# Kernel optimization log

Hardware: AMD Instinct MI355X
Metric: run time of the kernel (lower is better)

## Reference

```python
import jax, jax.numpy as jnp
import numpy as np

N, E = 50000, 800000
FN, FE, D, H = 64, 16, 128, 4


def setup_inputs() -> dict:
    key = jax.random.key(0)
    ks = jax.random.split(key, 16)
    inp = {
        "nodes": jax.random.normal(ks[0], (N, FN), jnp.float32),
        "edges": jax.random.normal(ks[1], (E, FE), jnp.float32),
        "senders": jax.random.randint(ks[2], (E,), 0, N, jnp.int32),
        "receivers": jax.random.randint(ks[3], (E,), 0, N, jnp.int32),
        "avg_multi_head": 0,
        # params (orthogonal init approximated by scaled normal; math identical)
        "W_node": jax.random.normal(ks[4], (FN, D), jnp.float32) / np.sqrt(FN),
        "b_node": jnp.zeros((D,), jnp.float32),
        "W_edge": jax.random.normal(ks[5], (FE, D), jnp.float32) / np.sqrt(FE),
        "b_edge": jnp.zeros((D,), jnp.float32),
        "Wk_s": jax.random.normal(ks[6], (H, D, D), jnp.float32) / np.sqrt(D),
        "bk_s": jnp.zeros((H, D), jnp.float32),
        "Wk_r": jax.random.normal(ks[7], (H, D, D), jnp.float32) / np.sqrt(D),
        "bk_r": jnp.zeros((H, D), jnp.float32),
        "W_out": jax.random.normal(ks[8], (H * D, D), jnp.float32) / np.sqrt(H * D),
        "b_out": jnp.zeros((D,), jnp.float32),
    }
    return inp


def _segment_softmax(logits, seg_ids, num_segments):
    seg_max = jax.ops.segment_max(logits, seg_ids, num_segments=num_segments)
    seg_max = jnp.where(jnp.isfinite(seg_max), seg_max, 0.0)  # empty segments
    e = jnp.exp(logits - seg_max[seg_ids])
    seg_sum = jax.ops.segment_sum(e, seg_ids, num_segments=num_segments)
    return e / seg_sum[seg_ids]


def reference(nodes, edges, senders, receivers, avg_multi_head,
              W_node, b_node, W_edge, b_edge, Wk_s, bk_s, Wk_r, bk_r,
              W_out, b_out):
    n_node = nodes.shape[0]
    x = nodes @ W_node + b_node            # [N, D] projected nodes
    ef = edges @ W_edge + b_edge           # [E, D] projected edge features
    sa = x[senders]                        # [E, D] sent attributes
    ra = x[receivers]                      # [E, D] received attributes
    scale = 1.0 / jnp.sqrt(jnp.asarray(D, x.dtype))
    heads = []
    for h in range(H):  # small fixed head count, structurally distinct params
        k_s = sa @ Wk_s[h] + bk_s[h]                 # [E, D]
        k_r = ra @ Wk_r[h] + bk_r[h] + ef            # [E, D]
        logits = jnp.sum(k_s * k_r, axis=1) * scale  # [E]
        w = _segment_softmax(logits, receivers, n_node)
        msg = w[:, None] * (sa + ef)                 # [E, D]
        heads.append(jax.ops.segment_sum(msg, receivers, num_segments=n_node))
    if avg_multi_head:
        agg = jnp.mean(jnp.stack(heads), axis=0)
    else:
        agg = jnp.concatenate(heads, axis=1) @ W_out + b_out
    return jax.nn.relu(x + agg)            # new node features [N, D]
```

## Files before the change

### kernel.cpp

```cpp
#include <hip/hip_runtime.h>

typedef unsigned short u16;
typedef unsigned int u32;
typedef short bh8 __attribute__((ext_vector_type(8)));
typedef float f4 __attribute__((ext_vector_type(4)));
typedef float pf2 __attribute__((ext_vector_type(2)));

__device__ __forceinline__ float bf2f(u16 h) { return __uint_as_float(((u32)h) << 16); }
__device__ __forceinline__ float bflo(u32 u) { return __uint_as_float(u << 16); }
__device__ __forceinline__ float bfhi(u32 u) { return __uint_as_float(u & 0xffff0000u); }
__device__ __forceinline__ u16 f2bf(float f) {
    u32 x = __float_as_uint(f);
    return (u16)((x + 0x7fffu + ((x >> 16) & 1u)) >> 16);
}
__device__ __forceinline__ pf2 pkfma(pf2 a, pf2 b, pf2 c) {
    pf2 d;
    asm("v_pk_fma_f32 %0, %1, %2, %3" : "=v"(d) : "v"(a), "v"(b), "v"(c));
    return d;
}
__device__ __forceinline__ pf2 u2f2(u32 u) {
    pf2 r;
    r.x = bflo(u);
    r.y = bfhi(u);
    return r;
}
__device__ __forceinline__ float dpp_red16(float x) {
    int y;
    y = __builtin_amdgcn_update_dpp(0, __float_as_int(x), 0xB1, 0xF, 0xF, true);
    x += __int_as_float(y);
    y = __builtin_amdgcn_update_dpp(0, __float_as_int(x), 0x4E, 0xF, 0xF, true);
    x += __int_as_float(y);
    y = __builtin_amdgcn_update_dpp(0, __float_as_int(x), 0x141, 0xF, 0xF, true);
    x += __int_as_float(y);
    y = __builtin_amdgcn_update_dpp(0, __float_as_int(x), 0x140, 0xF, 0xF, true);
    x += __int_as_float(y);
    return x;
}

#define KSCL 0.12751744336457488f

__global__ void k0a_kernel(const float* __restrict__ Wn, const float* __restrict__ Wks,
                           const float* __restrict__ Wkr, float* __restrict__ A,
                           float* __restrict__ B) {
    int idx = blockIdx.x * 256 + threadIdx.x;
    if (idx >= 65536) return;
    int which = idx >> 15;
    int rem = idx & 32767;
    int h = rem >> 13;
    int r = rem & 8191;
    int a = r >> 7, dp = r & 127;
    const float* W = which ? Wks : Wkr;
    float acc = 0.f;
    for (int d = 0; d < 128; ++d)
        acc += Wn[a * 128 + d] * W[(h * 128 + d) * 128 + dp];
    (which ? B : A)[(h * 64 + a) * 128 + dp] = acc;
}

__global__ void k0a2_kernel(const float* __restrict__ bn, const float* __restrict__ Wks,
                            const float* __restrict__ Wkr, const float* __restrict__ bks,
                            const float* __restrict__ bkr, float* __restrict__ ybs,
                            float* __restrict__ ybr) {
    int idx = blockIdx.x * 256 + threadIdx.x;
    if (idx >= 1024) return;
    int which = idx >> 9;
    int rem = idx & 511;
    int h = rem >> 7, dp = rem & 127;
    const float* W = which ? Wks : Wkr;
    const float* b = which ? bks : bkr;
    float acc = b[h * 128 + dp];
    for (int d = 0; d < 128; ++d) acc += bn[d] * W[(h * 128 + d) * 128 + dp];
    (which ? ybs : ybr)[h * 128 + dp] = acc;
}

__global__ void k0b_kernel(const float* __restrict__ Wn, const float* __restrict__ bn,
                           const float* __restrict__ A, const float* __restrict__ B,
                           const float* __restrict__ ybr, const float* __restrict__ ybs,
                           const float* __restrict__ Wks, const float* __restrict__ Wedge,
                           const float* __restrict__ bks, const float* __restrict__ bedge,
                           float* __restrict__ Wfold, float* __restrict__ biasrow) {
    int idx = blockIdx.x * 256 + threadIdx.x;
    if (idx >= 65 * 708) return;
    int a = idx / 708, c = idx % 708;
    float val;
    if (c < 128) {
        val = (a < 64) ? Wn[a * 128 + c] : bn[c];
    } else if (c < 640) {
        int h = (c - 128) >> 7, i = (c - 128) & 127;
        const float* rv = (a < 64) ? &A[(h * 64 + a) * 128] : &ybr[h * 128];
        float s = 0.f;
        for (int d = 0; d < 128; ++d) s += rv[d] * Wks[(h * 128 + i) * 128 + d];
        val = s;
    } else if (c < 704) {
        int k = (c - 640) >> 2, h = (c - 640) & 3;
        const float* rv = (a < 64) ? &B[(h * 64 + a) * 128] : &ybs[h * 128];
        float s = 0.f;
        for (int d = 0; d < 128; ++d) s += rv[d] * Wedge[k * 128 + d];
        val = s;
    } else {
        int h = c - 704;
        const float* rv = (a < 64) ? &B[(h * 64 + a) * 128] : &ybs[h * 128];
        float s = 0.f;
        for (int d = 0; d < 128; ++d) s += rv[d] * bedge[d];
        val = s;
    }
    if (a < 64) Wfold[(size_t)a * 708 + c] = val;
    else biasrow[c] = val;
}

__global__ void wconv_kernel(const float* __restrict__ Wfold, const float* __restrict__ Wout,
                             u16* __restrict__ WfT, u16* __restrict__ WoT) {
    int i = blockIdx.x * 256 + threadIdx.x;
    if (i < 768 * 64) {
        int c = i >> 6, k = i & 63;
        WfT[i] = f2bf(c < 708 ? Wfold[(size_t)k * 708 + c] : 0.f);
    }
    int j = i - 768 * 64;
    if (j >= 0 && j < 128 * 512) {
        int c = j >> 9, k = j & 511;
        WoT[j] = f2bf(Wout[(size_t)k * 128 + c]);
    }
}

__global__ __launch_bounds__(256) void g1_kernel(const float* __restrict__ nodes,
                                                 const u16* __restrict__ WfT,
                                                 const float* __restrict__ biasrow,
                                                 u16* __restrict__ Xc, u16* __restrict__ V,
                                                 u16* __restrict__ U, float* __restrict__ E0,
                                                 int N) {
    __shared__ u16 Asm[64][72];
    __shared__ u16 Bsm[128][72];
    int t = threadIdx.x;
    int r0 = blockIdx.x * 64, c0 = blockIdx.y * 128;
    {
        int row = t >> 2, cb = (t & 3) * 16;
        int r = r0 + row;
        u16 pk[16];
        if (r < N) {
            const float* src = &nodes[(size_t)r * 64 + cb];
#pragma unroll
            for (int q = 0; q < 16; ++q) pk[q] = f2bf(src[q]);
        } else {
#pragma unroll
            for (int q = 0; q < 16; ++q) pk[q] = 0;
        }
        *(uint4*)&Asm[row][cb] = *(const uint4*)&pk[0];
        *(uint4*)&Asm[row][cb + 8] = *(const uint4*)&pk[8];
    }
    {
        int col = t >> 1, ks = (t & 1) * 32;
        const u16* src = &WfT[(size_t)(c0 + col) * 64 + ks];
        uint4 v0 = *(const uint4*)src;
        uint4 v1 = *(const uint4*)(src + 8);
        uint4 v2 = *(const uint4*)(src + 16);
        uint4 v3 = *(const uint4*)(src + 24);
        *(uint4*)&Bsm[col][ks] = v0;
        *(uint4*)&Bsm[col][ks + 8] = v1;
        *(uint4*)&Bsm[col][ks + 16] = v2;
        *(uint4*)&Bsm[col][ks + 24] = v3;
    }
    __syncthreads();
    int lane = t & 63, wave = t >> 6;
    int wm = wave >> 1, wn = wave & 1;
    int lr = lane & 15, lk = lane >> 4;
    f4 acc[2][4] = {};
#pragma unroll
    for (int kk = 0; kk < 2; ++kk) {
        bh8 a[2], b[4];
#pragma unroll
        for (int am = 0; am < 2; ++am)
            a[am] = *(const bh8*)&Asm[wm * 32 + am * 16 + lr][kk * 32 + lk * 8];
#pragma unroll
        for (int bn = 0; bn < 4; ++bn)
            b[bn] = *(const bh8*)&Bsm[wn * 64 + bn * 16 + lr][kk * 32 + lk * 8];
#pragma unroll
        for (int am = 0; am < 2; ++am)
#pragma unroll
            for (int bn = 0; bn < 4; ++bn)
                acc[am][bn] = __builtin_amdgcn_mfma_f32_16x16x32_bf16(a[am], b[bn], acc[am][bn], 0, 0, 0);
    }
#pragma unroll
    for (int am = 0; am < 2; ++am)
#pragma unroll
        for (int bn = 0; bn < 4; ++bn) {
            int c = c0 + wn * 64 + bn * 16 + lr;
            if (c < 708) {
                float brow = biasrow[c];
#pragma unroll
                for (int q = 0; q < 4; ++q) {
                    int r = r0 + wm * 32 + am * 16 + lk * 4 + q;
                    if (r < N) {
                        float val = acc[am][bn][q] + brow;
                        if (c < 128) Xc[(size_t)r * 128 + c] = f2bf(val);
                        else if (c < 640) V[(size_t)r * 512 + (c - 128)] = f2bf(val * KSCL);
                        else if (c < 704) U[(size_t)r * 64 + (c - 640)] = f2bf(val * KSCL);
                        else E0[(size_t)r * 4 + (c - 704)] = exp2f(val * KSCL);
                    }
                }
            }
        }
}

__global__ void hist_kernel(const int* __restrict__ recv, int* __restrict__ deg, int E) {
    int e = blockIdx.x * 256 + threadIdx.x;
    if (e < E) atomicAdd(&deg[recv[e]], 1);
}

__global__ __launch_bounds__(1024) void scan1_kernel(const int* __restrict__ deg,
                                                     int* __restrict__ pre,
                                                     int* __restrict__ bsum, int N) {
    __shared__ int sm[1024];
    int b = blockIdx.x, t = threadIdx.x;
    int i = b * 1024 + t;
    int v = (i < N) ? deg[i] : 0;
    sm[t] = v;
    __syncthreads();
    for (int off = 1; off < 1024; off <<= 1) {
        int u = (t >= off) ? sm[t - off] : 0;
        __syncthreads();
        sm[t] += u;
        __syncthreads();
    }
    if (i < N) pre[i] = sm[t] - v;
    if (t == 1023) bsum[b] = sm[1023];
}

__global__ void scan2_kernel(int* __restrict__ bsum, int* __restrict__ boff, int nb) {
    int t = threadIdx.x;
    int own = (t < nb) ? bsum[t] : 0;
    int v = own;
#pragma unroll
    for (int off = 1; off < 64; off <<= 1) {
        int u = __shfl_up(v, off);
        if (t >= off) v += u;
    }
    if (t < nb) boff[t] = v - own;
    if (t == 63) boff[64] = v;
}

__global__ void scan3_kernel(const int* __restrict__ pre, const int* __restrict__ boff,
                             int* __restrict__ row_start, int* __restrict__ cursor, int N) {
    int i = blockIdx.x * 1024 + threadIdx.x;
    if (i < N) {
        int rsv = pre[i] + boff[i >> 10];
        row_start[i] = rsv;
        cursor[i] = rsv;
    }
    if (i == N) row_start[N] = boff[64];
}

__global__ void scatter_kernel(const int* __restrict__ recv, const int* __restrict__ senders,
                               int* __restrict__ cursor, int2* __restrict__ esp, int E) {
    int e = blockIdx.x * 256 + threadIdx.x;
    if (e < E) {
        int s = senders[e];
        int p = atomicAdd(&cursor[recv[e]], 1);
        esp[p] = make_int2(e, s);
    }
}

__global__ __launch_bounds__(256, 4) void en_kernel(const int* __restrict__ row_start,
                                                    const int2* __restrict__ esp,
                                                    const float* __restrict__ edges,
                                                    const u16* __restrict__ Xc,
                                                    const u16* __restrict__ V,
                                                    const u16* __restrict__ Uu,
                                                    const float* __restrict__ E0,
                                                    const float* __restrict__ W_edge,
                                                    const float* __restrict__ b_edge,
                                                    u16* __restrict__ agg, int N) {
    __shared__ float Wl[2048];
    int t = threadIdx.x;
    for (int i = t; i < 2048; i += 256) {
        int k = i >> 7, ch = i & 127;
        int pos = (k << 7) | ((((ch >> 1) & 3) << 5) | (((ch >> 3) & 15) << 1) | (ch & 1));
        Wl[pos] = W_edge[i];
    }
    __syncthreads();
    int lane = t & 63, wid = t >> 6;
    int g = lane >> 4, k16 = lane & 15;
    int hp = wid & 1;
    int nw = blockIdx.x * 2 + (wid >> 1);
    int NW = gridDim.x * 2;

#define IDX8(ea, sa, eb, sb, s_)                                            \
    {                                                                       \
        int ev = 0, sv = 0;                                                 \
        if (lane < 8) {                                                     \
            int jj = (s_)*8 + lane;                                         \
            if (jj >= deg) jj = deg - 1;                                    \
            int2 pv = esp[rs + jj];                                         \
            ev = pv.x; sv = pv.y;                                           \
        }                                                                   \
        ea = __shfl(ev, g); sa = __shfl(sv, g);                             \
        eb = __shfl(ev, 4 + g); sb = __shfl(sv, 4 + g);                     \
    }

#define LOADP(Xq, Uq, Eq, Zq, eI, sI)                                       \
    {                                                                       \
        Xq = *(const uint4*)(Xc + (size_t)(sI)*128 + 8 * k16);              \
        Uq = *(const u32*)(Uu + (size_t)(sI)*64 + k16 * 4 + 2 * hp);        \
        Eq = edges[(size_t)(eI)*16 + k16];                                  \
        Zq = *(const float2*)(E0 + (size_t)(sI)*4 + 2 * hp);                \
    }

#define COMP(Xq, Uq, Eq, Zq, act)                                           \
    {                                                                       \
        pf2 X0 = u2f2(Xq.x), X1 = u2f2(Xq.y), X2 = u2f2(Xq.z), X3 = u2f2(Xq.w); \
        float uh0 = bflo(Uq), uh1 = bfhi(Uq);                               \
        pf2 p2 = {Eq * uh0, 0.f};                                           \
        p2 = pkfma(X0, v00, p2); p2 = pkfma(X1, v01, p2);                   \
        p2 = pkfma(X2, v02, p2); p2 = pkfma(X3, v03, p2);                   \
        float p = dpp_red16(p2.x + p2.y);                                   \
        float wh = (act) ? Zq.x * exp2f(p) : 0.f;                           \
        Ss0 += wh; aE0 = fmaf(wh, Eq, aE0);                                 \
        pf2 w2 = {wh, wh};                                                  \
        aX00 = pkfma(w2, X0, aX00); aX01 = pkfma(w2, X1, aX01);             \
        aX02 = pkfma(w2, X2, aX02); aX03 = pkfma(w2, X3, aX03);             \
        pf2 q2 = {Eq * uh1, 0.f};                                           \
        q2 = pkfma(X0, v10, q2); q2 = pkfma(X1, v11, q2);                   \
        q2 = pkfma(X2, v12, q2); q2 = pkfma(X3, v13, q2);                   \
        float q = dpp_red16(q2.x + q2.y);                                   \
        float wg = (act) ? Zq.y * exp2f(q) : 0.f;                           \
        Ss1 += wg; aE1 = fmaf(wg, Eq, aE1);                                 \
        pf2 g2 = {wg, wg};                                                  \
        aX10 = pkfma(g2, X0, aX10); aX11 = pkfma(g2, X1, aX11);             \
        aX12 = pkfma(g2, X2, aX12); aX13 = pkfma(g2, X3, aX13);             \
    }

    for (int n = nw; n < N; n += NW) {
        int rs = row_start[n];
        int deg = row_start[n + 1] - rs;
        const u16* Vr = V + (size_t)n * 512;
        pf2 v00, v01, v02, v03, v10, v11, v12, v13;
        {
            uint4 v = *(const uint4*)(Vr + (2 * hp) * 128 + 8 * k16);
            v00 = u2f2(v.x); v01 = u2f2(v.y); v02 = u2f2(v.z); v03 = u2f2(v.w);
            uint4 w = *(const uint4*)(Vr + (2 * hp + 1) * 128 + 8 * k16);
            v10 = u2f2(w.x); v11 = u2f2(w.y); v12 = u2f2(w.z); v13 = u2f2(w.w);
        }
        pf2 aX00 = {0.f, 0.f}, aX01 = {0.f, 0.f}, aX02 = {0.f, 0.f}, aX03 = {0.f, 0.f};
        pf2 aX10 = {0.f, 0.f}, aX11 = {0.f, 0.f}, aX12 = {0.f, 0.f}, aX13 = {0.f, 0.f};
        float Ss0 = 0.f, Ss1 = 0.f, aE0 = 0.f, aE1 = 0.f;

        if (deg > 0) {
            int nst = (deg + 7) >> 3;
            int eA0, sA0, eA1, sA1, eB0, sB0, eB1, sB1;
            IDX8(eA0, sA0, eA1, sA1, 0);
            uint4 xP0, xP1; u32 uP0, uP1; float eP0, eP1; float2 zP0, zP1;
            LOADP(xP0, uP0, eP0, zP0, eA0, sA0);
            LOADP(xP1, uP1, eP1, zP1, eA1, sA1);
            if (nst > 1) {
                IDX8(eB0, sB0, eB1, sB1, 1);
            } else {
                eB0 = eA0; sB0 = sA0; eB1 = eA1; sB1 = sA1;
            }
            for (int s = 0; s < nst; ++s) {
                uint4 xc0 = xP0, xc1 = xP1;
                u32 uc0 = uP0, uc1 = uP1;
                float ec0 = eP0, ec1 = eP1;
                float2 zc0 = zP0, zc1 = zP1;
                int base = s * 8;
                if (s + 1 < nst) {
                    LOADP(xP0, uP0, eP0, zP0, eB0, sB0);
                    LOADP(xP1, uP1, eP1, zP1, eB1, sB1);
                    if (s + 2 < nst) IDX8(eB0, sB0, eB1, sB1, s + 2);
                }
                COMP(xc0, uc0, ec0, zc0, base + g < deg);
                COMP(xc1, uc1, ec1, zc1, base + 4 + g < deg);
            }
        }
#pragma unroll
        for (int msk = 16; msk <= 32; msk <<= 1) {
            aX00.x += __shfl_xor(aX00.x, msk); aX00.y += __shfl_xor(aX00.y, msk);
            aX01.x += __shfl_xor(aX01.x, msk); aX01.y += __shfl_xor(aX01.y, msk);
            aX02.x += __shfl_xor(aX02.x, msk); aX02.y += __shfl_xor(aX02.y, msk);
            aX03.x += __shfl_xor(aX03.x, msk); aX03.y += __shfl_xor(aX03.y, msk);
            aX10.x += __shfl_xor(aX10.x, msk); aX10.y += __shfl_xor(aX10.y, msk);
            aX11.x += __shfl_xor(aX11.x, msk); aX11.y += __shfl_xor(aX11.y, msk);
            aX12.x += __shfl_xor(aX12.x, msk); aX12.y += __shfl_xor(aX12.y, msk);
            aX13.x += __shfl_xor(aX13.x, msk); aX13.y += __shfl_xor(aX13.y, msk);
            Ss0 += __shfl_xor(Ss0, msk); Ss1 += __shfl_xor(Ss1, msk);
            aE0 += __shfl_xor(aE0, msk); aE1 += __shfl_xor(aE1, msk);
        }
        int hsel = g >> 1;
        int kh = (g & 1) << 3;
        bool prim = (g & 1) == 0;
        pf2 z = {0.f, 0.f};
        pf2 axg0 = prim ? (hsel ? aX10 : aX00) : z;
        pf2 axg1 = prim ? (hsel ? aX11 : aX01) : z;
        pf2 axg2 = prim ? (hsel ? aX12 : aX02) : z;
        pf2 axg3 = prim ? (hsel ? aX13 : aX03) : z;
        float aEg = hsel ? aE1 : aE0;
        float Sg = hsel ? Ss1 : Ss0;
        const pf2* Wp = (const pf2*)Wl;
#pragma unroll
        for (int kk = 0; kk < 8; ++kk) {
            int k = kh + kk;
            float a = __shfl(aEg, (lane & 48) | k);
            pf2 a2 = {a, a};
            int base = (k << 6) + k16;
            axg0 = pkfma(a2, Wp[base], axg0);
            axg1 = pkfma(a2, Wp[base + 16], axg1);
            axg2 = pkfma(a2, Wp[base + 32], axg2);
            axg3 = pkfma(a2, Wp[base + 48], axg3);
        }
        axg0.x += __shfl_xor(axg0.x, 16); axg0.y += __shfl_xor(axg0.y, 16);
        axg1.x += __shfl_xor(axg1.x, 16); axg1.y += __shfl_xor(axg1.y, 16);
        axg2.x += __shfl_xor(axg2.x, 16); axg2.y += __shfl_xor(axg2.y, 16);
        axg3.x += __shfl_xor(axg3.x, 16); axg3.y += __shfl_xor(axg3.y, 16);
        if (prim) {
            float inv = (deg > 0 && Sg > 0.f) ? 1.f / Sg : 0.f;
            float bes = (deg > 0) ? 1.f : 0.f;
            const float* br = &b_edge[8 * k16];
            u32 o0 = (u32)f2bf(axg0.x * inv + bes * br[0]) |
                     ((u32)f2bf(axg0.y * inv + bes * br[1]) << 16);
            u32 o1 = (u32)f2bf(axg1.x * inv + bes * br[2]) |
                     ((u32)f2bf(axg1.y * inv + bes * br[3]) << 16);
            u32 o2 = (u32)f2bf(axg2.x * inv + bes * br[4]) |
                     ((u32)f2bf(axg2.y * inv + bes * br[5]) << 16);
            u32 o3 = (u32)f2bf(axg3.x * inv + bes * br[6]) |
                     ((u32)f2bf(axg3.y * inv + bes * br[7]) << 16);
            uint4 st = {o0, o1, o2, o3};
            *(uint4*)(agg + (size_t)n * 512 + (2 * hp + hsel) * 128 + 8 * k16) = st;
        }
    }
#undef IDX8
#undef LOADP
#undef COMP
}

__global__ __launch_bounds__(256) void g3_kernel(const u16* __restrict__ Xc,
                                                 const u16* __restrict__ agg,
                                                 const u16* __restrict__ WoT,
                                                 const float* __restrict__ bout,
                                                 const int* __restrict__ avgflag,
                                                 float* __restrict__ out, int N) {
    int t = threadIdx.x;
    int r0 = blockIdx.x * 64;
    if (*avgflag) {
        for (int i = t; i < 64 * 128; i += 256) {
            int n = r0 + (i >> 7), j = i & 127;
            if (n < N) {
                float s = 0.f;
#pragma unroll
                for (int h = 0; h < 4; ++h) s += bf2f(agg[(size_t)n * 512 + h * 128 + j]);
                float v = bf2f(Xc[(size_t)n * 128 + j]) + 0.25f * s;
                out[(size_t)n * 128 + j] = v > 0.f ? v : 0.f;
            }
        }
        return;
    }
    __shared__ u16 Asm[64][72];
    __shared__ u16 Bsm[128][72];
    int lane = t & 63, wave = t >> 6;
    int wm = wave >> 1, wn = wave & 1;
    int lr = lane & 15, lk = lane >> 4;
    f4 acc[2][4] = {};
    for (int kb = 0; kb < 8; ++kb) {
        if (kb) __syncthreads();
        {
            int row = t >> 2, ks = (t & 3) * 16;
            int r = r0 + row;
            uint4 v0 = {0, 0, 0, 0}, v1 = {0, 0, 0, 0};
            if (r < N) {
                const u16* src = &agg[(size_t)r * 512 + kb * 64 + ks];
                v0 = *(const uint4*)src;
                v1 = *(const uint4*)(src + 8);
            }
            *(uint4*)&Asm[row][ks] = v0;
            *(uint4*)&Asm[row][ks + 8] = v1;
        }
        {
            int col = t >> 1, ks = (t & 1) * 32;
            const u16* src = &WoT[(size_t)col * 512 + kb * 64 + ks];
            uint4 v0 = *(const uint4*)src;
            uint4 v1 = *(const uint4*)(src + 8);
            uint4 v2 = *(const uint4*)(src + 16);
            uint4 v3 = *(const uint4*)(src + 24);
            *(uint4*)&Bsm[col][ks] = v0;
            *(uint4*)&Bsm[col][ks + 8] = v1;
            *(uint4*)&Bsm[col][ks + 16] = v2;
            *(uint4*)&Bsm[col][ks + 24] = v3;
        }
        __syncthreads();
#pragma unroll
        for (int kk = 0; kk < 2; ++kk) {
            bh8 a[2], b[4];
#pragma unroll
            for (int am = 0; am < 2; ++am)
                a[am] = *(const bh8*)&Asm[wm * 32 + am * 16 + lr][kk * 32 + lk * 8];
#pragma unroll
            for (int bn = 0; bn < 4; ++bn)
                b[bn] = *(const bh8*)&Bsm[wn * 64 + bn * 16 + lr][kk * 32 + lk * 8];
#pragma unroll
            for (int am = 0; am < 2; ++am)
#pragma unroll
                for (int bn = 0; bn < 4; ++bn)
                    acc[am][bn] = __builtin_amdgcn_mfma_f32_16x16x32_bf16(a[am], b[bn], acc[am][bn], 0, 0, 0);
        }
    }
#pragma unroll
    for (int am = 0; am < 2; ++am)
#pragma unroll
        for (int bn = 0; bn < 4; ++bn) {
            int c = wn * 64 + bn * 16 + lr;
            float bc = bout[c];
#pragma unroll
            for (int q = 0; q < 4; ++q) {
                int r = r0 + wm * 32 + am * 16 + lk * 4 + q;
                if (r < N) {
                    float v = acc[am][bn][q] + bc + bf2f(Xc[(size_t)r * 128 + c]);
                    out[(size_t)r * 128 + c] = v > 0.f ? v : 0.f;
                }
            }
        }
}

extern "C" void kernel_launch(void* const* d_in, const int* in_sizes, int n_in, void* d_out,
                              int out_size, void* d_ws, size_t ws_size, hipStream_t stream) {
    const float* nodes = (const float*)d_in[0];
    const float* edges = (const float*)d_in[1];
    const int* senders = (const int*)d_in[2];
    const int* receivers = (const int*)d_in[3];
    const int* avgflag = (const int*)d_in[4];
    const float* W_node = (const float*)d_in[5];
    const float* b_node = (const float*)d_in[6];
    const float* W_edge = (const float*)d_in[7];
    const float* b_edge = (const float*)d_in[8];
    const float* Wk_s = (const float*)d_in[9];
    const float* bk_s = (const float*)d_in[10];
    const float* Wk_r = (const float*)d_in[11];
    const float* bk_r = (const float*)d_in[12];
    const float* W_out = (const float*)d_in[13];
    const float* b_out = (const float*)d_in[14];
    int N = in_sizes[0] / 64;
    int E = in_sizes[2];
    float* outp = (float*)d_out;

    char* base = (char*)d_ws;
    size_t off = 0;
    auto alloc = [&](size_t nbytes) -> char* {
        char* p = base + off;
        off = (off + nbytes + 255) & ~(size_t)255;
        return p;
    };
    u16* Xc = (u16*)alloc((size_t)N * 128 * 2);
    u16* V = (u16*)alloc((size_t)N * 512 * 2);
    u16* U = (u16*)alloc((size_t)N * 64 * 2);
    float* E0 = (float*)alloc((size_t)N * 4 * 4);
    u16* agg = (u16*)alloc((size_t)N * 512 * 2);
    int* deg = (int*)alloc((size_t)N * 4);
    int* row_start = (int*)alloc((size_t)(N + 1) * 4);
    int* cursor = (int*)alloc((size_t)N * 4);
    int2* esp = (int2*)alloc((size_t)E * 8);
    int* pre = (int*)alloc((size_t)N * 4);
    int* bsum = (int*)alloc((size_t)128 * 4);
    int* boff = (int*)alloc((size_t)128 * 4);
    float* A = (float*)alloc((size_t)4 * 64 * 128 * 4);
    float* B = (float*)alloc((size_t)4 * 64 * 128 * 4);
    float* ybr = (float*)alloc((size_t)4 * 128 * 4);
    float* ybs = (float*)alloc((size_t)4 * 128 * 4);
    float* Wfold = (float*)alloc((size_t)64 * 708 * 4);
    float* biasrow = (float*)alloc((size_t)712 * 4);
    u16* WfT = (u16*)alloc((size_t)768 * 64 * 2);
    u16* WoT = (u16*)alloc((size_t)128 * 512 * 2);

    int nb = (N + 1023) >> 10;

    hipMemsetAsync(deg, 0, (size_t)N * 4, stream);
    k0a_kernel<<<256, 256, 0, stream>>>(W_node, Wk_s, Wk_r, A, B);
    k0a2_kernel<<<4, 256, 0, stream>>>(b_node, Wk_s, Wk_r, bk_s, bk_r, ybs, ybr);
    k0b_kernel<<<(65 * 708 + 255) / 256, 256, 0, stream>>>(W_node, b_node, A, B, ybr, ybs,
                                                           Wk_s, W_edge, bk_s, b_edge, Wfold,
                                                           biasrow);
    wconv_kernel<<<(768 * 64 + 128 * 512 + 255) / 256, 256, 0, stream>>>(Wfold, W_out, WfT, WoT);
    dim3 g1grid((N + 63) / 64, 6);
    g1_kernel<<<g1grid, 256, 0, stream>>>(nodes, WfT, biasrow, Xc, V, U, E0, N);
    hist_kernel<<<(E + 255) / 256, 256, 0, stream>>>(receivers, deg, E);
    scan1_kernel<<<nb, 1024, 0, stream>>>(deg, pre, bsum, N);
    scan2_kernel<<<1, 64, 0, stream>>>(bsum, boff, nb);
    scan3_kernel<<<(N + 1024) / 1024, 1024, 0, stream>>>(pre, boff, row_start, cursor, N);
    scatter_kernel<<<(E + 255) / 256, 256, 0, stream>>>(receivers, senders, cursor, esp, E);
    en_kernel<<<4096, 256, 0, stream>>>(row_start, esp, edges, Xc, V, U, E0, W_edge,
                                        b_edge, agg, N);
    g3_kernel<<<(N + 63) / 64, 256, 0, stream>>>(Xc, agg, WoT, b_out, avgflag, outp, N);
}
```

Baseline: 350.1 us.

## Process all four heads per wave instead of splitting head pairs across waves

The edge-to-node attention kernel now assigns one node per wave covering all four heads, where before two waves split the heads two and two. This halves redundant gathers of the sender features, edge features and index loads, and removes the prim-lane masking in the final edge-weight projection. In exchange each wave carries twice the accumulators and V registers, so launch bounds drop from 4 to 3 blocks per CU, which lowers occupancy for a latency-bound gather kernel.

```diff
diff --git a/kernel.cpp b/kernel.cpp
--- a/kernel.cpp
+++ b/kernel.cpp
@@ -258,7 +258,7 @@
     }
 }
 
-__global__ __launch_bounds__(256, 4) void en_kernel(const int* __restrict__ row_start,
+__global__ __launch_bounds__(256, 3) void en_kernel(const int* __restrict__ row_start,
                                                     const int2* __restrict__ esp,
                                                     const float* __restrict__ edges,
                                                     const u16* __restrict__ Xc,
@@ -278,9 +278,8 @@
     __syncthreads();
     int lane = t & 63, wid = t >> 6;
     int g = lane >> 4, k16 = lane & 15;
-    int hp = wid & 1;
-    int nw = blockIdx.x * 2 + (wid >> 1);
-    int NW = gridDim.x * 2;
+    int nw = blockIdx.x * 4 + wid;
+    int NW = gridDim.x * 4;
 
 #define IDX8(ea, sa, eb, sb, s_)                                            \
     {                                                                       \
@@ -298,55 +297,51 @@
 #define LOADP(Xq, Uq, Eq, Zq, eI, sI)                                       \
     {                                                                       \
         Xq = *(const uint4*)(Xc + (size_t)(sI)*128 + 8 * k16);              \
-        Uq = *(const u32*)(Uu + (size_t)(sI)*64 + k16 * 4 + 2 * hp);        \
+        Uq = *(const uint2*)(Uu + (size_t)(sI)*64 + k16 * 4);               \
         Eq = edges[(size_t)(eI)*16 + k16];                                  \
-        Zq = *(const float2*)(E0 + (size_t)(sI)*4 + 2 * hp);                \
+        Zq = *(const float4*)(E0 + (size_t)(sI)*4);                         \
     }
 
 #define COMP(Xq, Uq, Eq, Zq, act)                                           \
     {                                                                       \
         pf2 X0 = u2f2(Xq.x), X1 = u2f2(Xq.y), X2 = u2f2(Xq.z), X3 = u2f2(Xq.w); \
-        float uh0 = bflo(Uq), uh1 = bfhi(Uq);                               \
-        pf2 p2 = {Eq * uh0, 0.f};                                           \
-        p2 = pkfma(X0, v00, p2); p2 = pkfma(X1, v01, p2);                   \
-        p2 = pkfma(X2, v02, p2); p2 = pkfma(X3, v03, p2);                   \
-        float p = dpp_red16(p2.x + p2.y);                                   \
-        float wh = (act) ? Zq.x * exp2f(p) : 0.f;                           \
-        Ss0 += wh; aE0 = fmaf(wh, Eq, aE0);                                 \
-        pf2 w2 = {wh, wh};                                                  \
-        aX00 = pkfma(w2, X0, aX00); aX01 = pkfma(w2, X1, aX01);             \
-        aX02 = pkfma(w2, X2, aX02); aX03 = pkfma(w2, X3, aX03);             \
-        pf2 q2 = {Eq * uh1, 0.f};                                           \
-        q2 = pkfma(X0, v10, q2); q2 = pkfma(X1, v11, q2);                   \
-        q2 = pkfma(X2, v12, q2); q2 = pkfma(X3, v13, q2);                   \
-        float q = dpp_red16(q2.x + q2.y);                                   \
-        float wg = (act) ? Zq.y * exp2f(q) : 0.f;                           \
-        Ss1 += wg; aE1 = fmaf(wg, Eq, aE1);                                 \
-        pf2 g2 = {wg, wg};                                                  \
-        aX10 = pkfma(g2, X0, aX10); aX11 = pkfma(g2, X1, aX11);             \
-        aX12 = pkfma(g2, X2, aX12); aX13 = pkfma(g2, X3, aX13);             \
+        float uh[4] = {bflo(Uq.x), bfhi(Uq.x), bflo(Uq.y), bfhi(Uq.y)};     \
+        float e0a[4] = {Zq.x, Zq.y, Zq.z, Zq.w};                            \
+        _Pragma("unroll") for (int h = 0; h < 4; ++h) {                     \
+            pf2 p2 = {Eq * uh[h], 0.f};                                     \
+            p2 = pkfma(X0, vr[h][0], p2); p2 = pkfma(X1, vr[h][1], p2);     \
+            p2 = pkfma(X2, vr[h][2], p2); p2 = pkfma(X3, vr[h][3], p2);     \
+            float p = dpp_red16(p2.x + p2.y);                               \
+            float wh = (act) ? e0a[h] * exp2f(p) : 0.f;                     \
+            Ss[h] += wh; aE[h] = fmaf(wh, Eq, aE[h]);                       \
+            pf2 w2 = {wh, wh};                                              \
+            aX[h][0] = pkfma(w2, X0, aX[h][0]);                             \
+            aX[h][1] = pkfma(w2, X1, aX[h][1]);                             \
+            aX[h][2] = pkfma(w2, X2, aX[h][2]);                             \
+            aX[h][3] = pkfma(w2, X3, aX[h][3]);                             \
+        }                                                                   \
     }
 
     for (int n = nw; n < N; n += NW) {
         int rs = row_start[n];
         int deg = row_start[n + 1] - rs;
         const u16* Vr = V + (size_t)n * 512;
-        pf2 v00, v01, v02, v03, v10, v11, v12, v13;
-        {
-            uint4 v = *(const uint4*)(Vr + (2 * hp) * 128 + 8 * k16);
-            v00 = u2f2(v.x); v01 = u2f2(v.y); v02 = u2f2(v.z); v03 = u2f2(v.w);
-            uint4 w = *(const uint4*)(Vr + (2 * hp + 1) * 128 + 8 * k16);
-            v10 = u2f2(w.x); v11 = u2f2(w.y); v12 = u2f2(w.z); v13 = u2f2(w.w);
-        }
-        pf2 aX00 = {0.f, 0.f}, aX01 = {0.f, 0.f}, aX02 = {0.f, 0.f}, aX03 = {0.f, 0.f};
-        pf2 aX10 = {0.f, 0.f}, aX11 = {0.f, 0.f}, aX12 = {0.f, 0.f}, aX13 = {0.f, 0.f};
-        float Ss0 = 0.f, Ss1 = 0.f, aE0 = 0.f, aE1 = 0.f;
+        pf2 vr[4][4];
+#pragma unroll
+        for (int h = 0; h < 4; ++h) {
+            uint4 v = *(const uint4*)(Vr + h * 128 + 8 * k16);
+            vr[h][0] = u2f2(v.x); vr[h][1] = u2f2(v.y);
+            vr[h][2] = u2f2(v.z); vr[h][3] = u2f2(v.w);
+        }
+        pf2 aX[4][4] = {};
+        float Ss[4] = {0.f, 0.f, 0.f, 0.f};
+        float aE[4] = {0.f, 0.f, 0.f, 0.f};
 
         if (deg > 0) {
             int nst = (deg + 7) >> 3;
             int eA0, sA0, eA1, sA1, eB0, sB0, eB1, sB1;
             IDX8(eA0, sA0, eA1, sA1, 0);
-            uint4 xP0, xP1; u32 uP0, uP1; float eP0, eP1; float2 zP0, zP1;
+            uint4 xP0, xP1; uint2 uP0, uP1; float eP0, eP1; float4 zP0, zP1;
             LOADP(xP0, uP0, eP0, zP0, eA0, sA0);
             LOADP(xP1, uP1, eP1, zP1, eA1, sA1);
             if (nst > 1) {
@@ -356,9 +351,9 @@
             }
             for (int s = 0; s < nst; ++s) {
                 uint4 xc0 = xP0, xc1 = xP1;
-                u32 uc0 = uP0, uc1 = uP1;
+                uint2 uc0 = uP0, uc1 = uP1;
                 float ec0 = eP0, ec1 = eP1;
-                float2 zc0 = zP0, zc1 = zP1;
+                float4 zc0 = zP0, zc1 = zP1;
                 int base = s * 8;
                 if (s + 1 < nst) {
                     LOADP(xP0, uP0, eP0, zP0, eB0, sB0);
@@ -370,58 +365,48 @@
             }
         }
 #pragma unroll
-        for (int msk = 16; msk <= 32; msk <<= 1) {
-            aX00.x += __shfl_xor(aX00.x, msk); aX00.y += __shfl_xor(aX00.y, msk);
-            aX01.x += __shfl_xor(aX01.x, msk); aX01.y += __shfl_xor(aX01.y, msk);
-            aX02.x += __shfl_xor(aX02.x, msk); aX02.y += __shfl_xor(aX02.y, msk);
-            aX03.x += __shfl_xor(aX03.x, msk); aX03.y += __shfl_xor(aX03.y, msk);
-            aX10.x += __shfl_xor(aX10.x, msk); aX10.y += __shfl_xor(aX10.y, msk);
-            aX11.x += __shfl_xor(aX11.x, msk); aX11.y += __shfl_xor(aX11.y, msk);
-            aX12.x += __shfl_xor(aX12.x, msk); aX12.y += __shfl_xor(aX12.y, msk);
-            aX13.x += __shfl_xor(aX13.x, msk); aX13.y += __shfl_xor(aX13.y, msk);
-            Ss0 += __shfl_xor(Ss0, msk); Ss1 += __shfl_xor(Ss1, msk);
-            aE0 += __shfl_xor(aE0, msk); aE1 += __shfl_xor(aE1, msk);
-        }
-        int hsel = g >> 1;
-        int kh = (g & 1) << 3;
-        bool prim = (g & 1) == 0;
-        pf2 z = {0.f, 0.f};
-        pf2 axg0 = prim ? (hsel ? aX10 : aX00) : z;
-        pf2 axg1 = prim ? (hsel ? aX11 : aX01) : z;
-        pf2 axg2 = prim ? (hsel ? aX12 : aX02) : z;
-        pf2 axg3 = prim ? (hsel ? aX13 : aX03) : z;
-        float aEg = hsel ? aE1 : aE0;
-        float Sg = hsel ? Ss1 : Ss0;
+        for (int h = 0; h < 4; ++h) {
+#pragma unroll
+            for (int i = 0; i < 4; ++i) {
+                pf2 v = aX[h][i];
+                v.x += __shfl_xor(v.x, 16); v.y += __shfl_xor(v.y, 16);
+                v.x += __shfl_xor(v.x, 32); v.y += __shfl_xor(v.y, 32);
+                aX[h][i] = v;
+            }
+            Ss[h] += __shfl_xor(Ss[h], 16); Ss[h] += __shfl_xor(Ss[h], 32);
+            aE[h] += __shfl_xor(aE[h], 16); aE[h] += __shfl_xor(aE[h], 32);
+        }
+        pf2 axg[4];
+#pragma unroll
+        for (int i = 0; i < 4; ++i)
+            axg[i] = g == 0 ? aX[0][i] : g == 1 ? aX[1][i] : g == 2 ? aX[2][i] : aX[3][i];
+        float aEg = g == 0 ? aE[0] : g == 1 ? aE[1] : g == 2 ? aE[2] : aE[3];
+        float Sg = g == 0 ? Ss[0] : g == 1 ? Ss[1] : g == 2 ? Ss[2] : Ss[3];
         const pf2* Wp = (const pf2*)Wl;
 #pragma unroll
-        for (int kk = 0; kk < 8; ++kk) {
-            int k = kh + kk;
-            float a = __shfl(aEg, (lane & 48) | k);
+        for (int kk = 0; kk < 16; ++kk) {
+            float a = __shfl(aEg, (g << 4) | kk);
             pf2 a2 = {a, a};
-            int base = (k << 6) + k16;
-            axg0 = pkfma(a2, Wp[base], axg0);
-            axg1 = pkfma(a2, Wp[base + 16], axg1);
-            axg2 = pkfma(a2, Wp[base + 32], axg2);
-            axg3 = pkfma(a2, Wp[base + 48], axg3);
-        }
-        axg0.x += __shfl_xor(axg0.x, 16); axg0.y += __shfl_xor(axg0.y, 16);
-        axg1.x += __shfl_xor(axg1.x, 16); axg1.y += __shfl_xor(axg1.y, 16);
-        axg2.x += __shfl_xor(axg2.x, 16); axg2.y += __shfl_xor(axg2.y, 16);
-        axg3.x += __shfl_xor(axg3.x, 16); axg3.y += __shfl_xor(axg3.y, 16);
-        if (prim) {
+            int base = (kk << 6) + k16;
+            axg[0] = pkfma(a2, Wp[base], axg[0]);
+            axg[1] = pkfma(a2, Wp[base + 16], axg[1]);
+            axg[2] = pkfma(a2, Wp[base + 32], axg[2]);
+            axg[3] = pkfma(a2, Wp[base + 48], axg[3]);
+        }
+        {
             float inv = (deg > 0 && Sg > 0.f) ? 1.f / Sg : 0.f;
             float bes = (deg > 0) ? 1.f : 0.f;
             const float* br = &b_edge[8 * k16];
-            u32 o0 = (u32)f2bf(axg0.x * inv + bes * br[0]) |
-                     ((u32)f2bf(axg0.y * inv + bes * br[1]) << 16);
-            u32 o1 = (u32)f2bf(axg1.x * inv + bes * br[2]) |
-                     ((u32)f2bf(axg1.y * inv + bes * br[3]) << 16);
-            u32 o2 = (u32)f2bf(axg2.x * inv + bes * br[4]) |
-                     ((u32)f2bf(axg2.y * inv + bes * br[5]) << 16);
-            u32 o3 = (u32)f2bf(axg3.x * inv + bes * br[6]) |
-                     ((u32)f2bf(axg3.y * inv + bes * br[7]) << 16);
+            u32 o0 = (u32)f2bf(axg[0].x * inv + bes * br[0]) |
+                     ((u32)f2bf(axg[0].y * inv + bes * br[1]) << 16);
+            u32 o1 = (u32)f2bf(axg[1].x * inv + bes * br[2]) |
+                     ((u32)f2bf(axg[1].y * inv + bes * br[3]) << 16);
+            u32 o2 = (u32)f2bf(axg[2].x * inv + bes * br[4]) |
+                     ((u32)f2bf(axg[2].y * inv + bes * br[5]) << 16);
+            u32 o3 = (u32)f2bf(axg[3].x * inv + bes * br[6]) |
+                     ((u32)f2bf(axg[3].y * inv + bes * br[7]) << 16);
             uint4 st = {o0, o1, o2, o3};
-            *(uint4*)(agg + (size_t)n * 512 + (2 * hp + hsel) * 128 + 8 * k16) = st;
+            *(uint4*)(agg + (size_t)n * 512 + g * 128 + 8 * k16) = st;
         }
     }
 #undef IDX8
```

After: 331.0 us. 5.5% less time.
